# Kernel tuning notes

Hardware: AMD Instinct MI355X
Metric: run time of the kernel (lower is better)

## Reference

```python
import jax, jax.numpy as jnp
import numpy as np

B, C, H, W = 256, 512, 8, 32
A = 512          # attention channels
HID = 512        # GRU hidden size
NC = 97          # num_class
T = 26           # num_steps
IN = C + NC      # GRU input size (attention feat ++ one-hot text)


def setup_inputs() -> dict:
    key = jax.random.key(0)
    ks = jax.random.split(key, 12)
    s = 0.02
    return {
        "feats": jax.random.normal(ks[0], (B, C, H, W), jnp.float32),
        "texts": jax.random.randint(ks[1], (B, T), 0, NC),
        "embeddings": jnp.eye(NC, dtype=jnp.float32),  # diag(ones(num_class)) buffer
        # input attention block: 1x1 convs == dense over channel dim
        "Wf": jax.random.normal(ks[2], (A, C), jnp.float32) * s,   # feat 1x1 conv
        "bf": jnp.zeros((A,), jnp.float32),
        "Wh": jax.random.normal(ks[3], (A, HID), jnp.float32) * s, # hidden 1x1 conv
        "bh": jnp.zeros((A,), jnp.float32),
        "ws": jax.random.normal(ks[4], (A,), jnp.float32) * s,     # score 1x1 conv (A->1)
        # GRU cell (torch GRUCell layout: 3*HID rows ordered r,z,n)
        "W_ih": jax.random.normal(ks[5], (3 * HID, IN), jnp.float32) * s,
        "b_ih": jnp.zeros((3 * HID,), jnp.float32),
        "W_hh": jax.random.normal(ks[6], (3 * HID, HID), jnp.float32) * s,
        "b_hh": jnp.zeros((3 * HID,), jnp.float32),
        # generator linear
        "Wg": jax.random.normal(ks[7], (NC, HID), jnp.float32) * s,
        "bg": jnp.zeros((NC,), jnp.float32),
    }


def reference(feats, texts, embeddings, Wf, bf, Wh, bh, ws, W_ih, b_ih, W_hh, b_hh, Wg, bg):
    # Precompute feat branch of the attention block (identical each step): [B,A,H,W]
    feat_x = jnp.einsum('bchw,ac->bahw', feats, Wf) + bf[None, :, None, None]

    def step(h, idx):
        text_feat = embeddings[idx]                              # [B,NC] one-hot lookup
        hq = h @ Wh.T + bh                                       # [B,A] (1x1 conv on hidden)
        e = jnp.tanh(feat_x + hq[:, :, None, None])              # [B,A,H,W]
        score = jnp.einsum('bahw,a->bhw', e, ws)                 # [B,H,W]
        alpha = jax.nn.softmax(score.reshape(score.shape[0], -1), axis=1)
        alpha = alpha.reshape(score.shape)                        # spatial softmax
        attn_feat = jnp.einsum('bchw,bhw->bc', feats, alpha)     # [B,C]
        x = jnp.concatenate([attn_feat, text_feat], axis=1)      # [B,IN]
        # GRU cell
        gi = x @ W_ih.T + b_ih
        gh = h @ W_hh.T + b_hh
        i_r, i_z, i_n = jnp.split(gi, 3, axis=1)
        h_r, h_z, h_n = jnp.split(gh, 3, axis=1)
        r = jax.nn.sigmoid(i_r + h_r)
        z = jax.nn.sigmoid(i_z + h_z)
        n = jnp.tanh(i_n + r * h_n)
        h_new = (1.0 - z) * n + z * h
        out = h_new @ Wg.T + bg                                   # generator
        return h_new, out

    h0 = jnp.zeros((feats.shape[0], HID), feats.dtype)            # cell.init_hidden
    _, outs = jax.lax.scan(step, h0, texts.T)                     # teacher forcing (training)
    return jnp.transpose(outs, (1, 0, 2))                         # [B,T,NC]
```

## Files before the change

kernel.cpp:

```cpp
#include <hip/hip_runtime.h>

#define BB   256
#define CC   512
#define HWSZ 256
#define AA   512
#define HID  512
#define NCLS 97
#define TT   26
#define OUTW (TT*NCLS)
#define NWC  2176

typedef unsigned short u16;
typedef u16   u16x8 __attribute__((ext_vector_type(8)));
typedef short s16x8 __attribute__((ext_vector_type(8)));
typedef float f32x4 __attribute__((ext_vector_type(4)));

__device__ __forceinline__ u16 f2bf(float f){
  union { float f; unsigned int u; } v; v.f = f;
  unsigned int u = v.u;
  return (u16)((u + 0x7fffu + ((u>>16)&1u)) >> 16);
}
__device__ __forceinline__ float bf2f(u16 h){
  union { unsigned int u; float f; } v; v.u = ((unsigned int)h)<<16;
  return v.f;
}
__device__ __forceinline__ float tanh_fast(float x){
  float p = __expf(2.0f*x);
  return 1.0f - 2.0f*__builtin_amdgcn_rcpf(p + 1.0f);
}
__device__ __forceinline__ float sigmoid_f(float x){
  return 1.0f/(1.0f + __expf(-x));
}

__global__ __launch_bounds__(256) void wprep(
    const float* __restrict__ W_hh, const float* __restrict__ Wh,
    const float* __restrict__ Wg, const float* __restrict__ W_ih,
    const float* __restrict__ Wf,
    u16* __restrict__ Wc_hi, u16* __restrict__ Wc_lo,
    u16* __restrict__ Wih_hi, u16* __restrict__ Wih_lo,
    u16* __restrict__ Wf_bf,
    float* __restrict__ hbuf, u16* __restrict__ h_hi, u16* __restrict__ h_lo)
{
  int r = blockIdx.x, t = threadIdx.x;
  if (r < NWC){
    #pragma unroll
    for (int cc=0; cc<2; cc++){
      int c = t + cc*256;
      float v = 0.f;
      if (r < 1536)      v = W_hh[(size_t)r*512 + c];
      else if (r < 2048) v = Wh[(size_t)(r-1536)*512 + c];
      else if (r < 2145) v = Wg[(size_t)(r-2048)*512 + c];
      u16 hi = f2bf(v); u16 lo = f2bf(v - bf2f(hi));
      Wc_hi[(size_t)r*512 + c] = hi;
      Wc_lo[(size_t)r*512 + c] = lo;
      if (r < 512) Wf_bf[(size_t)r*512 + c] = f2bf(Wf[(size_t)r*512 + c]);
    }
  } else if (r < 3712){
    int rr = r - NWC;
    #pragma unroll
    for (int cc=0; cc<2; cc++){
      int c = t + cc*256;
      float v = W_ih[(size_t)rr*609 + c];
      u16 hi = f2bf(v); u16 lo = f2bf(v - bf2f(hi));
      Wih_hi[(size_t)rr*512 + c] = hi;
      Wih_lo[(size_t)rr*512 + c] = lo;
    }
  } else {
    int bb = r - 3712;
    #pragma unroll
    for (int cc=0; cc<2; cc++){
      int c = t + cc*256;
      hbuf[(size_t)bb*512 + c] = 0.f;
      h_hi[(size_t)bb*512 + c] = 0;
      h_lo[(size_t)bb*512 + c] = 0;
    }
  }
}

__global__ __launch_bounds__(256) void prep_kernel(
    const float* __restrict__ feats, u16* __restrict__ feats_t)
{
  int b = blockIdx.x, t = threadIdx.x;
  #pragma unroll
  for (int cc=0; cc<2; cc++){
    int c = t + cc*256;
    const float4* src = (const float4*)(feats + ((size_t)b*CC + c)*HWSZ);
    u16* dst = feats_t + (size_t)b*HWSZ*CC + c;
    for (int q=0; q<HWSZ/4; q++){
      float4 v = src[q];
      dst[(size_t)(q*4+0)*CC] = f2bf(v.x);
      dst[(size_t)(q*4+1)*CC] = f2bf(v.y);
      dst[(size_t)(q*4+2)*CC] = f2bf(v.z);
      dst[(size_t)(q*4+3)*CC] = f2bf(v.w);
    }
  }
}

__global__ __launch_bounds__(256,2) void featx_gemm(
    const u16* __restrict__ Wf_bf, const u16* __restrict__ feats_t,
    const float* __restrict__ bfv, u16* __restrict__ feat_x)
{
  int b = blockIdx.z;
  int a0 = blockIdx.y*128, hw0 = blockIdx.x*128;
  __shared__ u16 As[128*64];
  __shared__ u16 Bs[128*64];
  int tid = threadIdx.x, lane = tid&63;
  int wm = tid>>7, wn = (tid>>6)&1;

  f32x4 acc[4][4];
  #pragma unroll
  for (int m=0;m<4;m++)
    #pragma unroll
    for (int n=0;n<4;n++)
      #pragma unroll
      for (int j=0;j<4;j++) acc[m][n][j]=0.f;

  const u16* gA = Wf_bf + (size_t)a0*CC;
  const u16* gB = feats_t + ((size_t)b*HWSZ + hw0)*CC;

  for (int kk=0; kk<CC; kk+=64){
    #pragma unroll
    for (int i=0;i<4;i++){
      int s = tid + i*256;
      int row = s>>3, ce = (s&7)*8;
      int phys = row*64 + (ce ^ ((row&7)*8));
      *(u16x8*)(As + phys) = *(const u16x8*)(gA + (size_t)row*CC + kk + ce);
      *(u16x8*)(Bs + phys) = *(const u16x8*)(gB + (size_t)row*CC + kk + ce);
    }
    __syncthreads();
    #pragma unroll
    for (int h=0; h<2; h++){
      s16x8 af[4], bfr[4];
      #pragma unroll
      for (int m=0;m<4;m++){
        int row = wm*64 + m*16 + (lane&15);
        int ce  = h*32 + (lane>>4)*8;
        af[m] = *(const s16x8*)(As + row*64 + (ce ^ ((row&7)*8)));
      }
      #pragma unroll
      for (int n=0;n<4;n++){
        int row = wn*64 + n*16 + (lane&15);
        int ce  = h*32 + (lane>>4)*8;
        bfr[n] = *(const s16x8*)(Bs + row*64 + (ce ^ ((row&7)*8)));
      }
      #pragma unroll
      for (int m=0;m<4;m++)
        #pragma unroll
        for (int n=0;n<4;n++)
          acc[m][n] = __builtin_amdgcn_mfma_f32_16x16x32_bf16(af[m], bfr[n], acc[m][n], 0, 0, 0);
    }
    __syncthreads();
  }
  #pragma unroll
  for (int m=0;m<4;m++){
    int arb = wm*64 + m*16 + ((lane>>4)<<2);
    #pragma unroll
    for (int n=0;n<4;n++){
      int hw = hw0 + wn*64 + n*16 + (lane&15);
      u16* dst = feat_x + ((size_t)b*HWSZ + hw)*AA;
      #pragma unroll
      for (int j=0;j<4;j++){
        int ar = a0 + arb + j;
        dst[ar] = f2bf(acc[m][n][j] + bfv[ar]);
      }
    }
  }
}

__global__ __launch_bounds__(256) void hstep(
    const u16* __restrict__ h_hi, const u16* __restrict__ h_lo,
    const u16* __restrict__ Wc_hi, const u16* __restrict__ Wc_lo,
    const float* __restrict__ b_hh, const float* __restrict__ bhv,
    const float* __restrict__ bgv, float* __restrict__ ghq,
    float* __restrict__ dout, int t, int ntoff)
{
  int tid = threadIdx.x, lane = tid&63, wv = tid>>6;
  int n0 = (blockIdx.x + ntoff)*64, m0 = blockIdx.y*64 + wv*16;
  int lr = lane & 15, koff = (lane>>4)*8;

  const u16* pah = h_hi + (size_t)(m0+lr)*512 + koff;
  const u16* pal = h_lo + (size_t)(m0+lr)*512 + koff;
  const u16* pbh[4]; const u16* pbl[4];
  #pragma unroll
  for (int f=0; f<4; f++){
    pbh[f] = Wc_hi + (size_t)(n0 + f*16 + lr)*512 + koff;
    pbl[f] = Wc_lo + (size_t)(n0 + f*16 + lr)*512 + koff;
  }

  f32x4 acc[4];
  #pragma unroll
  for (int f=0;f<4;f++)
    #pragma unroll
    for (int j=0;j<4;j++) acc[f][j]=0.f;

  #pragma unroll
  for (int c=0; c<16; c++){
    int ko = c*32;
    s16x8 ah = *(const s16x8*)(pah + ko);
    s16x8 al = *(const s16x8*)(pal + ko);
    #pragma unroll
    for (int f=0; f<4; f++){
      s16x8 bh = *(const s16x8*)(pbh[f] + ko);
      s16x8 bl = *(const s16x8*)(pbl[f] + ko);
      acc[f] = __builtin_amdgcn_mfma_f32_16x16x32_bf16(ah, bh, acc[f], 0,0,0);
      acc[f] = __builtin_amdgcn_mfma_f32_16x16x32_bf16(ah, bl, acc[f], 0,0,0);
      acc[f] = __builtin_amdgcn_mfma_f32_16x16x32_bf16(al, bh, acc[f], 0,0,0);
    }
  }

  int mrow = m0 + (lane>>4)*4;
  #pragma unroll
  for (int f=0; f<4; f++){
    int col = n0 + f*16 + lr;
    #pragma unroll
    for (int j=0; j<4; j++){
      float v = acc[f][j];
      int row = mrow + j;
      if (col < 1536)      ghq[(size_t)row*2048 + col] = v + b_hh[col];
      else if (col < 2048) ghq[(size_t)row*2048 + col] = v + bhv[col-1536];
      else if (col < 2145){
        if (t > 0) dout[(size_t)row*OUTW + (size_t)(t-1)*NCLS + (col-2048)] = v + bgv[col-2048];
      }
    }
  }
}

__global__ __launch_bounds__(256) void gi_gemm(
    const u16* __restrict__ at_hi, const u16* __restrict__ at_lo,
    const u16* __restrict__ Wih_hi, const u16* __restrict__ Wih_lo,
    const float* __restrict__ b_ih, float* __restrict__ gi)
{
  int tid = threadIdx.x, lane = tid&63, wv = tid>>6;
  int n0 = blockIdx.x*64, m0 = blockIdx.y*64 + wv*16;
  int lr = lane & 15, koff = (lane>>4)*8;

  const u16* pah = at_hi + (size_t)(m0+lr)*512 + koff;
  const u16* pal = at_lo + (size_t)(m0+lr)*512 + koff;
  const u16* pbh[4]; const u16* pbl[4];
  #pragma unroll
  for (int f=0; f<4; f++){
    pbh[f] = Wih_hi + (size_t)(n0 + f*16 + lr)*512 + koff;
    pbl[f] = Wih_lo + (size_t)(n0 + f*16 + lr)*512 + koff;
  }

  f32x4 acc[4];
  #pragma unroll
  for (int f=0;f<4;f++)
    #pragma unroll
    for (int j=0;j<4;j++) acc[f][j]=0.f;

  #pragma unroll
  for (int c=0; c<16; c++){
    int ko = c*32;
    s16x8 ah = *(const s16x8*)(pah + ko);
    s16x8 al = *(const s16x8*)(pal + ko);
    #pragma unroll
    for (int f=0; f<4; f++){
      s16x8 bh = *(const s16x8*)(pbh[f] + ko);
      s16x8 bl = *(const s16x8*)(pbl[f] + ko);
      acc[f] = __builtin_amdgcn_mfma_f32_16x16x32_bf16(ah, bh, acc[f], 0,0,0);
      acc[f] = __builtin_amdgcn_mfma_f32_16x16x32_bf16(ah, bl, acc[f], 0,0,0);
      acc[f] = __builtin_amdgcn_mfma_f32_16x16x32_bf16(al, bh, acc[f], 0,0,0);
    }
  }

  int mrow = m0 + (lane>>4)*4;
  #pragma unroll
  for (int f=0; f<4; f++){
    int col = n0 + f*16 + lr;
    #pragma unroll
    for (int j=0; j<4; j++){
      int row = mrow + j;
      gi[(size_t)row*1536 + col] = acc[f][j] + b_ih[col];
    }
  }
}

__global__ __launch_bounds__(1024) void attn_kernel(
    const u16* __restrict__ feat_x, const u16* __restrict__ feats_t,
    const float* __restrict__ ghq, const float* __restrict__ wsv,
    u16* __restrict__ at_hi, u16* __restrict__ at_lo)
{
  int b = blockIdx.x, t = threadIdx.x;
  int w = t>>6, lane = t&63;
  __shared__ float hq_s[512], ws_s[512], sc_s[256], red[8];
  __shared__ float part[16][512];
  if (t < 512){
    hq_s[t] = ghq[(size_t)b*2048 + 1536 + t];
    ws_s[t] = wsv[t];
  }
  __syncthreads();

  float hql[8], wsl[8];
  #pragma unroll
  for (int j=0;j<8;j++){ hql[j]=hq_s[lane*8+j]; wsl[j]=ws_s[lane*8+j]; }

  const u16* fxb = feat_x + (size_t)b*HWSZ*AA;
  int rbase = w*16;
  #pragma unroll
  for (int k=0;k<16;k+=4){
    int r0 = rbase + k;
    u16x8 v0 = *(const u16x8*)(fxb + (size_t)(r0  )*512 + lane*8);
    u16x8 v1 = *(const u16x8*)(fxb + (size_t)(r0+1)*512 + lane*8);
    u16x8 v2 = *(const u16x8*)(fxb + (size_t)(r0+2)*512 + lane*8);
    u16x8 v3 = *(const u16x8*)(fxb + (size_t)(r0+3)*512 + lane*8);
    float s0=0.f, s1=0.f, s2=0.f, s3=0.f;
    #pragma unroll
    for (int j=0;j<8;j++){
      s0 += tanh_fast(bf2f(v0[j]) + hql[j])*wsl[j];
      s1 += tanh_fast(bf2f(v1[j]) + hql[j])*wsl[j];
      s2 += tanh_fast(bf2f(v2[j]) + hql[j])*wsl[j];
      s3 += tanh_fast(bf2f(v3[j]) + hql[j])*wsl[j];
    }
    #pragma unroll
    for (int o=32;o;o>>=1){
      s0 += __shfl_xor(s0,o); s1 += __shfl_xor(s1,o);
      s2 += __shfl_xor(s2,o); s3 += __shfl_xor(s3,o);
    }
    if (lane==0){ sc_s[r0]=s0; sc_s[r0+1]=s1; sc_s[r0+2]=s2; sc_s[r0+3]=s3; }
  }
  __syncthreads();

  float sc=0.f, m=0.f, ex=0.f;
  if (t < 256){
    sc = sc_s[t]; m = sc;
    #pragma unroll
    for (int o=32;o;o>>=1) m = fmaxf(m, __shfl_xor(m,o));
    if (lane==0) red[w] = m;
  }
  __syncthreads();
  if (t < 256){
    m = fmaxf(fmaxf(red[0],red[1]), fmaxf(red[2],red[3]));
    ex = __expf(sc - m);
    float sm = ex;
    #pragma unroll
    for (int o=32;o;o>>=1) sm += __shfl_xor(sm,o);
    if (lane==0) red[4+w] = sm;
  }
  __syncthreads();
  if (t < 256){
    float sm = (red[4]+red[5])+(red[6]+red[7]);
    sc_s[t] = ex/sm;
  }
  __syncthreads();

  const u16* ftb = feats_t + (size_t)b*HWSZ*CC;
  float acc[8];
  #pragma unroll
  for (int j=0;j<8;j++) acc[j]=0.f;
  #pragma unroll
  for (int k=0;k<16;k+=4){
    int r0 = rbase + k;
    u16x8 v0 = *(const u16x8*)(ftb + (size_t)(r0  )*512 + lane*8);
    u16x8 v1 = *(const u16x8*)(ftb + (size_t)(r0+1)*512 + lane*8);
    u16x8 v2 = *(const u16x8*)(ftb + (size_t)(r0+2)*512 + lane*8);
    u16x8 v3 = *(const u16x8*)(ftb + (size_t)(r0+3)*512 + lane*8);
    float a0 = sc_s[r0], a1 = sc_s[r0+1], a2 = sc_s[r0+2], a3 = sc_s[r0+3];
    #pragma unroll
    for (int j=0;j<8;j++)
      acc[j] += (bf2f(v0[j])*a0 + bf2f(v1[j])*a1) + (bf2f(v2[j])*a2 + bf2f(v3[j])*a3);
  }
  #pragma unroll
  for (int j=0;j<8;j++) part[w][lane*8+j] = acc[j];
  __syncthreads();

  if (t < 512){
    float v = 0.f;
    #pragma unroll
    for (int q=0;q<16;q++) v += part[q][t];
    u16 hi = f2bf(v); u16 lo = f2bf(v - bf2f(hi));
    at_hi[(size_t)b*512+t]=hi; at_lo[(size_t)b*512+t]=lo;
  }
}

__global__ __launch_bounds__(256) void gate_kernel(
    const float* __restrict__ gi, const float* __restrict__ ghq,
    const float* __restrict__ W_ih, const int* __restrict__ texts,
    float* __restrict__ hbuf, u16* __restrict__ h_hi, u16* __restrict__ h_lo,
    int t)
{
  int b = blockIdx.x, tid = threadIdx.x;
  int idx = texts[b*TT + t];
  const float* gib = gi + (size_t)b*1536;
  const float* ghb = ghq + (size_t)b*2048;
  #pragma unroll
  for (int jj=0; jj<2; jj++){
    int j = tid + jj*256;
    float gir = gib[j]       + W_ih[(size_t)j*609        + 512 + idx];
    float giz = gib[512+j]   + W_ih[(size_t)(512+j)*609  + 512 + idx];
    float gin = gib[1024+j]  + W_ih[(size_t)(1024+j)*609 + 512 + idx];
    float r = sigmoid_f(gir + ghb[j]);
    float z = sigmoid_f(giz + ghb[512+j]);
    float n = tanh_fast(gin + r*ghb[1024+j]);
    float hv = hbuf[(size_t)b*512 + j];
    float hn = (1.f - z)*n + z*hv;
    hbuf[(size_t)b*512 + j] = hn;
    u16 hi = f2bf(hn); u16 lo = f2bf(hn - bf2f(hi));
    h_hi[(size_t)b*512 + j] = hi;
    h_lo[(size_t)b*512 + j] = lo;
  }
}

extern "C" void kernel_launch(void* const* d_in, const int* in_sizes, int n_in,
                              void* d_out, int out_size, void* d_ws, size_t ws_size,
                              hipStream_t stream) {
  const float* feats = (const float*)d_in[0];
  const int*   texts = (const int*)d_in[1];
  const float* Wf    = (const float*)d_in[3];
  const float* bfv   = (const float*)d_in[4];
  const float* Wh    = (const float*)d_in[5];
  const float* bh    = (const float*)d_in[6];
  const float* wsv   = (const float*)d_in[7];
  const float* W_ih  = (const float*)d_in[8];
  const float* b_ih  = (const float*)d_in[9];
  const float* W_hh  = (const float*)d_in[10];
  const float* b_hh  = (const float*)d_in[11];
  const float* Wg    = (const float*)d_in[12];
  const float* bg    = (const float*)d_in[13];
  float* dout = (float*)d_out;

  u16* feat_x = (u16*)d_in[0];

  const size_t NEED = 80478208;
  if (ws_size < NEED) return;

  char* w = (char*)d_ws;
  u16*   feats_t = (u16*)(w);
  u16*   Wf_bf   = (u16*)(w + 67108864);
  u16*   Wc_hi   = (u16*)(w + 67633152);
  u16*   Wc_lo   = (u16*)(w + 69861376);
  u16*   Wih_hi  = (u16*)(w + 72089600);
  u16*   Wih_lo  = (u16*)(w + 73662464);
  float* hbuf    = (float*)(w + 75235328);
  u16*   h_hi    = (u16*)(w + 75759616);
  u16*   h_lo    = (u16*)(w + 76021760);
  float* ghq     = (float*)(w + 76283904);
  u16*   at_hi   = (u16*)(w + 78381056);
  u16*   at_lo   = (u16*)(w + 78643200);
  float* gi      = (float*)(w + 78905344);

  wprep<<<3968, 256, 0, stream>>>(W_hh, Wh, Wg, W_ih, Wf,
                                  Wc_hi, Wc_lo, Wih_hi, Wih_lo, Wf_bf,
                                  hbuf, h_hi, h_lo);
  prep_kernel<<<BB, 256, 0, stream>>>(feats, feats_t);
  featx_gemm<<<dim3(2,4,BB), 256, 0, stream>>>(Wf_bf, feats_t, bfv, feat_x);

  for (int t=0; t<TT; t++){
    hstep<<<dim3(34,4), 256, 0, stream>>>(h_hi, h_lo, Wc_hi, Wc_lo,
                                          b_hh, bh, bg, ghq, dout, t, 0);
    attn_kernel<<<BB, 1024, 0, stream>>>(feat_x, feats_t, ghq, wsv, at_hi, at_lo);
    gi_gemm<<<dim3(24,4), 256, 0, stream>>>(at_hi, at_lo, Wih_hi, Wih_lo, b_ih, gi);
    gate_kernel<<<BB, 256, 0, stream>>>(gi, ghq, W_ih, texts, hbuf, h_hi, h_lo, t);
  }
  hstep<<<dim3(2,4), 256, 0, stream>>>(h_hi, h_lo, Wc_hi, Wc_lo,
                                       b_hh, bh, bg, ghq, dout, 26, 32);
}
```

Before: 2.197 ms.

## Fuse recurrent step loop into one persistent cooperative kernel with grid syncs

Replaces the 105 per-timestep launches (hstep, attn_kernel, gi_gemm, gate_kernel) with a single cooperative kernel of 256 blocks of 1024 threads. Each step's phases are separated by grid.sync(). The hidden GEMM tiles are spread across all waves of the grid. The input-gate GEMM is fused with the GRU gate math through shared memory, which removes the gi global buffer. This cuts launch gaps and one global round trip per step, at the cost of three grid-wide barriers per step and one 1024-thread block per CU.

```diff
diff --git a/kernel.cpp b/kernel.cpp
--- a/kernel.cpp
+++ b/kernel.cpp
@@ -1,4 +1,7 @@
 #include <hip/hip_runtime.h>
+#include <hip/hip_cooperative_groups.h>
+
+namespace cg = cooperative_groups;
 
 #define BB   256
 #define CC   512
@@ -167,237 +170,217 @@
   }
 }
 
-__global__ __launch_bounds__(256) void hstep(
-    const u16* __restrict__ h_hi, const u16* __restrict__ h_lo,
+__global__ __launch_bounds__(1024, 4) void fused_loop(
+    const u16* __restrict__ feat_x, const u16* __restrict__ feats_t,
     const u16* __restrict__ Wc_hi, const u16* __restrict__ Wc_lo,
+    const u16* __restrict__ Wih_hi, const u16* __restrict__ Wih_lo,
     const float* __restrict__ b_hh, const float* __restrict__ bhv,
-    const float* __restrict__ bgv, float* __restrict__ ghq,
-    float* __restrict__ dout, int t, int ntoff)
+    const float* __restrict__ bgv, const float* __restrict__ b_ih,
+    const float* __restrict__ wsv, const float* __restrict__ W_ih,
+    const int* __restrict__ texts,
+    float* __restrict__ hbuf, u16* __restrict__ h_hi, u16* __restrict__ h_lo,
+    float* __restrict__ ghq, u16* __restrict__ at_hi, u16* __restrict__ at_lo,
+    float* __restrict__ dout)
 {
-  int tid = threadIdx.x, lane = tid&63, wv = tid>>6;
-  int n0 = (blockIdx.x + ntoff)*64, m0 = blockIdx.y*64 + wv*16;
-  int lr = lane & 15, koff = (lane>>4)*8;
-
-  const u16* pah = h_hi + (size_t)(m0+lr)*512 + koff;
-  const u16* pal = h_lo + (size_t)(m0+lr)*512 + koff;
-  const u16* pbh[4]; const u16* pbl[4];
-  #pragma unroll
-  for (int f=0; f<4; f++){
-    pbh[f] = Wc_hi + (size_t)(n0 + f*16 + lr)*512 + koff;
-    pbl[f] = Wc_lo + (size_t)(n0 + f*16 + lr)*512 + koff;
-  }
-
-  f32x4 acc[4];
-  #pragma unroll
-  for (int f=0;f<4;f++)
-    #pragma unroll
-    for (int j=0;j<4;j++) acc[f][j]=0.f;
-
-  #pragma unroll
-  for (int c=0; c<16; c++){
-    int ko = c*32;
-    s16x8 ah = *(const s16x8*)(pah + ko);
-    s16x8 al = *(const s16x8*)(pal + ko);
-    #pragma unroll
-    for (int f=0; f<4; f++){
-      s16x8 bh = *(const s16x8*)(pbh[f] + ko);
-      s16x8 bl = *(const s16x8*)(pbl[f] + ko);
-      acc[f] = __builtin_amdgcn_mfma_f32_16x16x32_bf16(ah, bh, acc[f], 0,0,0);
-      acc[f] = __builtin_amdgcn_mfma_f32_16x16x32_bf16(ah, bl, acc[f], 0,0,0);
-      acc[f] = __builtin_amdgcn_mfma_f32_16x16x32_bf16(al, bh, acc[f], 0,0,0);
-    }
-  }
-
-  int mrow = m0 + (lane>>4)*4;
-  #pragma unroll
-  for (int f=0; f<4; f++){
-    int col = n0 + f*16 + lr;
-    #pragma unroll
-    for (int j=0; j<4; j++){
-      float v = acc[f][j];
-      int row = mrow + j;
-      if (col < 1536)      ghq[(size_t)row*2048 + col] = v + b_hh[col];
-      else if (col < 2048) ghq[(size_t)row*2048 + col] = v + bhv[col-1536];
-      else if (col < 2145){
-        if (t > 0) dout[(size_t)row*OUTW + (size_t)(t-1)*NCLS + (col-2048)] = v + bgv[col-2048];
-      }
-    }
-  }
-}
-
-__global__ __launch_bounds__(256) void gi_gemm(
-    const u16* __restrict__ at_hi, const u16* __restrict__ at_lo,
-    const u16* __restrict__ Wih_hi, const u16* __restrict__ Wih_lo,
-    const float* __restrict__ b_ih, float* __restrict__ gi)
-{
-  int tid = threadIdx.x, lane = tid&63, wv = tid>>6;
-  int n0 = blockIdx.x*64, m0 = blockIdx.y*64 + wv*16;
-  int lr = lane & 15, koff = (lane>>4)*8;
-
-  const u16* pah = at_hi + (size_t)(m0+lr)*512 + koff;
-  const u16* pal = at_lo + (size_t)(m0+lr)*512 + koff;
-  const u16* pbh[4]; const u16* pbl[4];
-  #pragma unroll
-  for (int f=0; f<4; f++){
-    pbh[f] = Wih_hi + (size_t)(n0 + f*16 + lr)*512 + koff;
-    pbl[f] = Wih_lo + (size_t)(n0 + f*16 + lr)*512 + koff;
-  }
-
-  f32x4 acc[4];
-  #pragma unroll
-  for (int f=0;f<4;f++)
-    #pragma unroll
-    for (int j=0;j<4;j++) acc[f][j]=0.f;
-
-  #pragma unroll
-  for (int c=0; c<16; c++){
-    int ko = c*32;
-    s16x8 ah = *(const s16x8*)(pah + ko);
-    s16x8 al = *(const s16x8*)(pal + ko);
-    #pragma unroll
-    for (int f=0; f<4; f++){
-      s16x8 bh = *(const s16x8*)(pbh[f] + ko);
-      s16x8 bl = *(const s16x8*)(pbl[f] + ko);
-      acc[f] = __builtin_amdgcn_mfma_f32_16x16x32_bf16(ah, bh, acc[f], 0,0,0);
-      acc[f] = __builtin_amdgcn_mfma_f32_16x16x32_bf16(ah, bl, acc[f], 0,0,0);
-      acc[f] = __builtin_amdgcn_mfma_f32_16x16x32_bf16(al, bh, acc[f], 0,0,0);
-    }
-  }
-
-  int mrow = m0 + (lane>>4)*4;
-  #pragma unroll
-  for (int f=0; f<4; f++){
-    int col = n0 + f*16 + lr;
-    #pragma unroll
-    for (int j=0; j<4; j++){
-      int row = mrow + j;
-      gi[(size_t)row*1536 + col] = acc[f][j] + b_ih[col];
-    }
-  }
-}
-
-__global__ __launch_bounds__(1024) void attn_kernel(
-    const u16* __restrict__ feat_x, const u16* __restrict__ feats_t,
-    const float* __restrict__ ghq, const float* __restrict__ wsv,
-    u16* __restrict__ at_hi, u16* __restrict__ at_lo)
-{
-  int b = blockIdx.x, t = threadIdx.x;
-  int w = t>>6, lane = t&63;
+  cg::grid_group grid = cg::this_grid();
+  const int blk = blockIdx.x, tid = threadIdx.x;
+  const int w = tid>>6, lane = tid&63;
+  const int lr = lane&15, koff = (lane>>4)*8;
+
   __shared__ float hq_s[512], ws_s[512], sc_s[256], red[8];
   __shared__ float part[16][512];
-  if (t < 512){
-    hq_s[t] = ghq[(size_t)b*2048 + 1536 + t];
-    ws_s[t] = wsv[t];
-  }
-  __syncthreads();
-
-  float hql[8], wsl[8];
-  #pragma unroll
-  for (int j=0;j<8;j++){ hql[j]=hq_s[lane*8+j]; wsl[j]=ws_s[lane*8+j]; }
-
-  const u16* fxb = feat_x + (size_t)b*HWSZ*AA;
-  int rbase = w*16;
-  #pragma unroll
-  for (int k=0;k<16;k+=4){
-    int r0 = rbase + k;
-    u16x8 v0 = *(const u16x8*)(fxb + (size_t)(r0  )*512 + lane*8);
-    u16x8 v1 = *(const u16x8*)(fxb + (size_t)(r0+1)*512 + lane*8);
-    u16x8 v2 = *(const u16x8*)(fxb + (size_t)(r0+2)*512 + lane*8);
-    u16x8 v3 = *(const u16x8*)(fxb + (size_t)(r0+3)*512 + lane*8);
-    float s0=0.f, s1=0.f, s2=0.f, s3=0.f;
-    #pragma unroll
-    for (int j=0;j<8;j++){
-      s0 += tanh_fast(bf2f(v0[j]) + hql[j])*wsl[j];
-      s1 += tanh_fast(bf2f(v1[j]) + hql[j])*wsl[j];
-      s2 += tanh_fast(bf2f(v2[j]) + hql[j])*wsl[j];
-      s3 += tanh_fast(bf2f(v3[j]) + hql[j])*wsl[j];
-    }
-    #pragma unroll
-    for (int o=32;o;o>>=1){
-      s0 += __shfl_xor(s0,o); s1 += __shfl_xor(s1,o);
-      s2 += __shfl_xor(s2,o); s3 += __shfl_xor(s3,o);
-    }
-    if (lane==0){ sc_s[r0]=s0; sc_s[r0+1]=s1; sc_s[r0+2]=s2; sc_s[r0+3]=s3; }
-  }
-  __syncthreads();
-
-  float sc=0.f, m=0.f, ex=0.f;
-  if (t < 256){
-    sc = sc_s[t]; m = sc;
-    #pragma unroll
-    for (int o=32;o;o>>=1) m = fmaxf(m, __shfl_xor(m,o));
-    if (lane==0) red[w] = m;
-  }
-  __syncthreads();
-  if (t < 256){
-    m = fmaxf(fmaxf(red[0],red[1]), fmaxf(red[2],red[3]));
-    ex = __expf(sc - m);
-    float sm = ex;
-    #pragma unroll
-    for (int o=32;o;o>>=1) sm += __shfl_xor(sm,o);
-    if (lane==0) red[4+w] = sm;
-  }
-  __syncthreads();
-  if (t < 256){
-    float sm = (red[4]+red[5])+(red[6]+red[7]);
-    sc_s[t] = ex/sm;
-  }
-  __syncthreads();
-
-  const u16* ftb = feats_t + (size_t)b*HWSZ*CC;
-  float acc[8];
-  #pragma unroll
-  for (int j=0;j<8;j++) acc[j]=0.f;
-  #pragma unroll
-  for (int k=0;k<16;k+=4){
-    int r0 = rbase + k;
-    u16x8 v0 = *(const u16x8*)(ftb + (size_t)(r0  )*512 + lane*8);
-    u16x8 v1 = *(const u16x8*)(ftb + (size_t)(r0+1)*512 + lane*8);
-    u16x8 v2 = *(const u16x8*)(ftb + (size_t)(r0+2)*512 + lane*8);
-    u16x8 v3 = *(const u16x8*)(ftb + (size_t)(r0+3)*512 + lane*8);
-    float a0 = sc_s[r0], a1 = sc_s[r0+1], a2 = sc_s[r0+2], a3 = sc_s[r0+3];
-    #pragma unroll
-    for (int j=0;j<8;j++)
-      acc[j] += (bf2f(v0[j])*a0 + bf2f(v1[j])*a1) + (bf2f(v2[j])*a2 + bf2f(v3[j])*a3);
-  }
-  #pragma unroll
-  for (int j=0;j<8;j++) part[w][lane*8+j] = acc[j];
-  __syncthreads();
-
-  if (t < 512){
-    float v = 0.f;
-    #pragma unroll
-    for (int q=0;q<16;q++) v += part[q][t];
-    u16 hi = f2bf(v); u16 lo = f2bf(v - bf2f(hi));
-    at_hi[(size_t)b*512+t]=hi; at_lo[(size_t)b*512+t]=lo;
-  }
-}
-
-__global__ __launch_bounds__(256) void gate_kernel(
-    const float* __restrict__ gi, const float* __restrict__ ghq,
-    const float* __restrict__ W_ih, const int* __restrict__ texts,
-    float* __restrict__ hbuf, u16* __restrict__ h_hi, u16* __restrict__ h_lo,
-    int t)
-{
-  int b = blockIdx.x, tid = threadIdx.x;
-  int idx = texts[b*TT + t];
-  const float* gib = gi + (size_t)b*1536;
-  const float* ghb = ghq + (size_t)b*2048;
-  #pragma unroll
-  for (int jj=0; jj<2; jj++){
-    int j = tid + jj*256;
-    float gir = gib[j]       + W_ih[(size_t)j*609        + 512 + idx];
-    float giz = gib[512+j]   + W_ih[(size_t)(512+j)*609  + 512 + idx];
-    float gin = gib[1024+j]  + W_ih[(size_t)(1024+j)*609 + 512 + idx];
-    float r = sigmoid_f(gir + ghb[j]);
-    float z = sigmoid_f(giz + ghb[512+j]);
-    float n = tanh_fast(gin + r*ghb[1024+j]);
-    float hv = hbuf[(size_t)b*512 + j];
-    float hn = (1.f - z)*n + z*hv;
-    hbuf[(size_t)b*512 + j] = hn;
-    u16 hi = f2bf(hn); u16 lo = f2bf(hn - bf2f(hi));
-    h_hi[(size_t)b*512 + j] = hi;
-    h_lo[(size_t)b*512 + j] = lo;
+  __shared__ float gis[3][16][32];
+
+  for (int t=0; t<=TT; t++){
+    {
+      int tile = w*256 + blk;
+      if (tile < 544){
+        int m0 = (tile & 15)*16;
+        int n0 = (tile >> 4)*64;
+        const u16* pah = h_hi + (size_t)(m0+lr)*512 + koff;
+        const u16* pal = h_lo + (size_t)(m0+lr)*512 + koff;
+        const u16* pbh[4]; const u16* pbl[4];
+        #pragma unroll
+        for (int f=0; f<4; f++){
+          pbh[f] = Wc_hi + (size_t)(n0 + f*16 + lr)*512 + koff;
+          pbl[f] = Wc_lo + (size_t)(n0 + f*16 + lr)*512 + koff;
+        }
+        f32x4 acc[4];
+        #pragma unroll
+        for (int f=0;f<4;f++)
+          #pragma unroll
+          for (int j=0;j<4;j++) acc[f][j]=0.f;
+        #pragma unroll
+        for (int c=0; c<16; c++){
+          int ko = c*32;
+          s16x8 ah = *(const s16x8*)(pah + ko);
+          s16x8 al = *(const s16x8*)(pal + ko);
+          #pragma unroll
+          for (int f=0; f<4; f++){
+            s16x8 bh = *(const s16x8*)(pbh[f] + ko);
+            s16x8 bl = *(const s16x8*)(pbl[f] + ko);
+            acc[f] = __builtin_amdgcn_mfma_f32_16x16x32_bf16(ah, bh, acc[f], 0,0,0);
+            acc[f] = __builtin_amdgcn_mfma_f32_16x16x32_bf16(ah, bl, acc[f], 0,0,0);
+            acc[f] = __builtin_amdgcn_mfma_f32_16x16x32_bf16(al, bh, acc[f], 0,0,0);
+          }
+        }
+        int mrow = m0 + (lane>>4)*4;
+        #pragma unroll
+        for (int f=0; f<4; f++){
+          int col = n0 + f*16 + lr;
+          #pragma unroll
+          for (int j=0; j<4; j++){
+            float v = acc[f][j];
+            int row = mrow + j;
+            if (col < 1536)      ghq[(size_t)row*2048 + col] = v + b_hh[col];
+            else if (col < 2048) ghq[(size_t)row*2048 + col] = v + bhv[col-1536];
+            else if (col < 2145){
+              if (t > 0) dout[(size_t)row*OUTW + (size_t)(t-1)*NCLS + (col-2048)] = v + bgv[col-2048];
+            }
+          }
+        }
+      }
+    }
+    if (t == TT) break;
+    grid.sync();
+
+    if (tid < 512){
+      hq_s[tid] = ghq[(size_t)blk*2048 + 1536 + tid];
+      ws_s[tid] = wsv[tid];
+    }
+    __syncthreads();
+
+    float hql[8], wsl[8];
+    #pragma unroll
+    for (int j=0;j<8;j++){ hql[j]=hq_s[lane*8+j]; wsl[j]=ws_s[lane*8+j]; }
+
+    const u16* fxb = feat_x + (size_t)blk*HWSZ*AA;
+    int rbase = w*16;
+    #pragma unroll
+    for (int k=0;k<16;k+=4){
+      int r0 = rbase + k;
+      u16x8 v0 = *(const u16x8*)(fxb + (size_t)(r0  )*512 + lane*8);
+      u16x8 v1 = *(const u16x8*)(fxb + (size_t)(r0+1)*512 + lane*8);
+      u16x8 v2 = *(const u16x8*)(fxb + (size_t)(r0+2)*512 + lane*8);
+      u16x8 v3 = *(const u16x8*)(fxb + (size_t)(r0+3)*512 + lane*8);
+      float s0=0.f, s1=0.f, s2=0.f, s3=0.f;
+      #pragma unroll
+      for (int j=0;j<8;j++){
+        s0 += tanh_fast(bf2f(v0[j]) + hql[j])*wsl[j];
+        s1 += tanh_fast(bf2f(v1[j]) + hql[j])*wsl[j];
+        s2 += tanh_fast(bf2f(v2[j]) + hql[j])*wsl[j];
+        s3 += tanh_fast(bf2f(v3[j]) + hql[j])*wsl[j];
+      }
+      #pragma unroll
+      for (int o=32;o;o>>=1){
+        s0 += __shfl_xor(s0,o); s1 += __shfl_xor(s1,o);
+        s2 += __shfl_xor(s2,o); s3 += __shfl_xor(s3,o);
+      }
+      if (lane==0){ sc_s[r0]=s0; sc_s[r0+1]=s1; sc_s[r0+2]=s2; sc_s[r0+3]=s3; }
+    }
+    __syncthreads();
+
+    float sc=0.f, m=0.f, ex=0.f;
+    if (tid < 256){
+      sc = sc_s[tid]; m = sc;
+      #pragma unroll
+      for (int o=32;o;o>>=1) m = fmaxf(m, __shfl_xor(m,o));
+      if (lane==0) red[w] = m;
+    }
+    __syncthreads();
+    if (tid < 256){
+      m = fmaxf(fmaxf(red[0],red[1]), fmaxf(red[2],red[3]));
+      ex = __expf(sc - m);
+      float sm = ex;
+      #pragma unroll
+      for (int o=32;o;o>>=1) sm += __shfl_xor(sm,o);
+      if (lane==0) red[4+w] = sm;
+    }
+    __syncthreads();
+    if (tid < 256){
+      float sm = (red[4]+red[5])+(red[6]+red[7]);
+      sc_s[tid] = ex/sm;
+    }
+    __syncthreads();
+
+    const u16* ftb = feats_t + (size_t)blk*HWSZ*CC;
+    float acc8[8];
+    #pragma unroll
+    for (int j=0;j<8;j++) acc8[j]=0.f;
+    #pragma unroll
+    for (int k=0;k<16;k+=4){
+      int r0 = rbase + k;
+      u16x8 v0 = *(const u16x8*)(ftb + (size_t)(r0  )*512 + lane*8);
+      u16x8 v1 = *(const u16x8*)(ftb + (size_t)(r0+1)*512 + lane*8);
+      u16x8 v2 = *(const u16x8*)(ftb + (size_t)(r0+2)*512 + lane*8);
+      u16x8 v3 = *(const u16x8*)(ftb + (size_t)(r0+3)*512 + lane*8);
+      float a0 = sc_s[r0], a1 = sc_s[r0+1], a2 = sc_s[r0+2], a3 = sc_s[r0+3];
+      #pragma unroll
+      for (int j=0;j<8;j++)
+        acc8[j] += (bf2f(v0[j])*a0 + bf2f(v1[j])*a1) + (bf2f(v2[j])*a2 + bf2f(v3[j])*a3);
+    }
+    #pragma unroll
+    for (int j=0;j<8;j++) part[w][lane*8+j] = acc8[j];
+    __syncthreads();
+
+    if (tid < 512){
+      float v = 0.f;
+      #pragma unroll
+      for (int q=0;q<16;q++) v += part[q][tid];
+      u16 hi = f2bf(v); u16 lo = f2bf(v - bf2f(hi));
+      at_hi[(size_t)blk*512+tid]=hi; at_lo[(size_t)blk*512+tid]=lo;
+    }
+    grid.sync();
+
+    {
+      int m0 = (blk >> 4)*16;
+      int j0 = (blk & 15)*32;
+      if (w < 6){
+        int g = w >> 1, hh2 = w & 1;
+        int nrow = g*512 + j0 + hh2*16;
+        const u16* pah = at_hi + (size_t)(m0+lr)*512 + koff;
+        const u16* pal = at_lo + (size_t)(m0+lr)*512 + koff;
+        const u16* pbh = Wih_hi + (size_t)(nrow+lr)*512 + koff;
+        const u16* pbl = Wih_lo + (size_t)(nrow+lr)*512 + koff;
+        f32x4 a4;
+        #pragma unroll
+        for (int j=0;j<4;j++) a4[j]=0.f;
+        #pragma unroll
+        for (int c=0; c<16; c++){
+          int ko = c*32;
+          s16x8 ah = *(const s16x8*)(pah + ko);
+          s16x8 al = *(const s16x8*)(pal + ko);
+          s16x8 bh = *(const s16x8*)(pbh + ko);
+          s16x8 bl = *(const s16x8*)(pbl + ko);
+          a4 = __builtin_amdgcn_mfma_f32_16x16x32_bf16(ah, bh, a4, 0,0,0);
+          a4 = __builtin_amdgcn_mfma_f32_16x16x32_bf16(ah, bl, a4, 0,0,0);
+          a4 = __builtin_amdgcn_mfma_f32_16x16x32_bf16(al, bh, a4, 0,0,0);
+        }
+        int orow = (lane>>4)*4;
+        #pragma unroll
+        for (int jj=0; jj<4; jj++) gis[g][orow+jj][hh2*16 + lr] = a4[jj];
+      }
+      __syncthreads();
+      if (tid < 512){
+        int r = tid>>5, c2 = tid&31;
+        int j = j0 + c2, brow = m0 + r;
+        int idx = texts[brow*TT + t];
+        float gir = gis[0][r][c2] + b_ih[j]       + W_ih[(size_t)j*609        + 512 + idx];
+        float giz = gis[1][r][c2] + b_ih[512+j]   + W_ih[(size_t)(512+j)*609  + 512 + idx];
+        float gin = gis[2][r][c2] + b_ih[1024+j]  + W_ih[(size_t)(1024+j)*609 + 512 + idx];
+        const float* ghb = ghq + (size_t)brow*2048;
+        float rg = sigmoid_f(gir + ghb[j]);
+        float zg = sigmoid_f(giz + ghb[512+j]);
+        float ng = tanh_fast(gin + rg*ghb[1024+j]);
+        float hv = hbuf[(size_t)brow*512 + j];
+        float hn = (1.f - zg)*ng + zg*hv;
+        hbuf[(size_t)brow*512 + j] = hn;
+        u16 hi = f2bf(hn); u16 lo = f2bf(hn - bf2f(hi));
+        h_hi[(size_t)brow*512 + j] = hi;
+        h_lo[(size_t)brow*512 + j] = lo;
+      }
+    }
+    grid.sync();
   }
 }
 
@@ -419,9 +402,10 @@
   const float* bg    = (const float*)d_in[13];
   float* dout = (float*)d_out;
 
-  u16* feat_x = (u16*)d_in[0];
-
-  const size_t NEED = 80478208;
+  const u16* feat_x = (const u16*)d_in[0];
+  u16* feat_x_w = (u16*)d_in[0];
+
+  const size_t NEED = 78905344;
   if (ws_size < NEED) return;
 
   char* w = (char*)d_ws;
@@ -437,21 +421,20 @@
   float* ghq     = (float*)(w + 76283904);
   u16*   at_hi   = (u16*)(w + 78381056);
   u16*   at_lo   = (u16*)(w + 78643200);
-  float* gi      = (float*)(w + 78905344);
 
   wprep<<<3968, 256, 0, stream>>>(W_hh, Wh, Wg, W_ih, Wf,
                                   Wc_hi, Wc_lo, Wih_hi, Wih_lo, Wf_bf,
                                   hbuf, h_hi, h_lo);
   prep_kernel<<<BB, 256, 0, stream>>>(feats, feats_t);
-  featx_gemm<<<dim3(2,4,BB), 256, 0, stream>>>(Wf_bf, feats_t, bfv, feat_x);
-
-  for (int t=0; t<TT; t++){
-    hstep<<<dim3(34,4), 256, 0, stream>>>(h_hi, h_lo, Wc_hi, Wc_lo,
-                                          b_hh, bh, bg, ghq, dout, t, 0);
-    attn_kernel<<<BB, 1024, 0, stream>>>(feat_x, feats_t, ghq, wsv, at_hi, at_lo);
-    gi_gemm<<<dim3(24,4), 256, 0, stream>>>(at_hi, at_lo, Wih_hi, Wih_lo, b_ih, gi);
-    gate_kernel<<<BB, 256, 0, stream>>>(gi, ghq, W_ih, texts, hbuf, h_hi, h_lo, t);
-  }
-  hstep<<<dim3(2,4), 256, 0, stream>>>(h_hi, h_lo, Wc_hi, Wc_lo,
-                                       b_hh, bh, bg, ghq, dout, 26, 32);
-}
+  featx_gemm<<<dim3(2,4,BB), 256, 0, stream>>>(Wf_bf, feats_t, bfv, feat_x_w);
+
+  void* args[] = {
+    (void*)&feat_x, (void*)&feats_t, (void*)&Wc_hi, (void*)&Wc_lo,
+    (void*)&Wih_hi, (void*)&Wih_lo, (void*)&b_hh, (void*)&bh, (void*)&bg,
+    (void*)&b_ih, (void*)&wsv, (void*)&W_ih, (void*)&texts,
+    (void*)&hbuf, (void*)&h_hi, (void*)&h_lo, (void*)&ghq,
+    (void*)&at_hi, (void*)&at_lo, (void*)&dout
+  };
+  hipLaunchCooperativeKernel(reinterpret_cast<void*>(fused_loop),
+                             dim3(BB), dim3(1024), args, 0, stream);
+}
```

Measured after the change: 5.194 ms. +136.4%, slower.
